# Optimization experiments

Measured on AMD Instinct MI355X. Metric: run time of the kernel, lower is better.

## Reference

```python
import jax, jax.numpy as jnp
import numpy as np

DEPTH, DIM, HEADS, DIM_HEAD, MLP = 6, 768, 12, 64, 3072
INNER = HEADS * DIM_HEAD  # 768
EPS = 1e-5


def _layernorm(x, w, b):
    m = jnp.mean(x, axis=-1, keepdims=True)
    v = jnp.mean((x - m) ** 2, axis=-1, keepdims=True)
    return (x - m) * jax.lax.rsqrt(v + EPS) * w + b


def setup_inputs() -> dict:
    key = jax.random.key(0)
    ks = jax.random.split(key, 12)
    s = 0.02
    return {
        "x": jax.random.normal(ks[0], (4, 1024, DIM), dtype=jnp.float32),
        "ln1_w": jnp.ones((DEPTH, DIM), jnp.float32),
        "ln1_b": jnp.zeros((DEPTH, DIM), jnp.float32),
        "w_qkv": jax.random.normal(ks[1], (DEPTH, DIM, 3 * INNER), jnp.float32) * s,
        "w_o": jax.random.normal(ks[2], (DEPTH, INNER, DIM), jnp.float32) * s,
        "b_o": jnp.zeros((DEPTH, DIM), jnp.float32),
        "ln2_w": jnp.ones((DEPTH, DIM), jnp.float32),
        "ln2_b": jnp.zeros((DEPTH, DIM), jnp.float32),
        "w1": jax.random.normal(ks[3], (DEPTH, DIM, MLP), jnp.float32) * s,
        "b1": jnp.zeros((DEPTH, MLP), jnp.float32),
        "w2": jax.random.normal(ks[4], (DEPTH, MLP, DIM), jnp.float32) * s,
        "b2": jnp.zeros((DEPTH, DIM), jnp.float32),
    }


def _forward(x, ln1_w, ln1_b, w_qkv, w_o, b_o, ln2_w, ln2_b, w1, b1, w2, b2):
    scale = DIM_HEAD ** -0.5
    b, n, _ = x.shape

    def block(x, p):
        l1w, l1b, wqkv, wo, bo, l2w, l2b, W1, B1, W2, B2 = p
        # --- attention (pre-norm); dropout/droppath are identity in eval ---
        h = _layernorm(x, l1w, l1b)
        qkv = h @ wqkv                                   # [b, n, 3*inner]
        q, k, v = jnp.split(qkv, 3, axis=-1)
        q = q.reshape(b, n, HEADS, DIM_HEAD).transpose(0, 2, 1, 3)
        k = k.reshape(b, n, HEADS, DIM_HEAD).transpose(0, 2, 1, 3)
        v = v.reshape(b, n, HEADS, DIM_HEAD).transpose(0, 2, 1, 3)
        dots = jnp.einsum('bhid,bhjd->bhij', q, k) * scale   # [b, h, n, n]
        attn = jax.nn.softmax(dots, axis=-1)
        out = jnp.einsum('bhij,bhjd->bhid', attn, v)
        out = out.transpose(0, 2, 1, 3).reshape(b, n, INNER)
        x = x + out @ wo + bo
        # --- feed-forward (pre-norm), exact GELU like torch default ---
        h = _layernorm(x, l2w, l2b)
        x = x + jax.nn.gelu(h @ W1 + B1, approximate=False) @ W2 + B2
        return x, None

    x, _ = jax.lax.scan(block, x, (ln1_w, ln1_b, w_qkv, w_o, b_o,
                                   ln2_w, ln2_b, w1, b1, w2, b2))
    return x


def reference(x, ln1_w, ln1_b, w_qkv, w_o, b_o, ln2_w, ln2_b, w1, b1, w2, b2):
    return _forward(x, ln1_w, ln1_b, w_qkv, w_o, b_o, ln2_w, ln2_b, w1, b1, w2, b2)
```

## Files before the change

### kernel.cpp

```cpp
#include <hip/hip_runtime.h>
#include <cmath>
#include <cstdint>

typedef __bf16 bf16_t;
typedef __bf16 bf16x8 __attribute__((ext_vector_type(8)));
typedef __bf16 bf16x4 __attribute__((ext_vector_type(4)));
typedef float  f32x4  __attribute__((ext_vector_type(4)));

#define DEPTH 6
#define DIM   768
#define HEADS 12
#define DH    64
#define MLPD  3072
#define SEQ   1024
#define BATCH 4
#define MTOT  (BATCH*SEQ)
#define QKVN  2304

static __device__ __forceinline__ bf16x8 ld8(const bf16_t* p) {
    return *(const bf16x8*)p;
}

typedef const __attribute__((address_space(1))) unsigned int gas_u32;
typedef __attribute__((address_space(3))) unsigned int las_u32;
static __device__ __forceinline__ void gload16(const bf16_t* g, bf16_t* l) {
    __builtin_amdgcn_global_load_lds((gas_u32*)g, (las_u32*)l, 16, 0, 0);
}

__global__ __launch_bounds__(256) void tcvt_kernel(const float* __restrict__ in,
                                                   bf16_t* __restrict__ out,
                                                   int K, int N) {
    __shared__ float ts[32][33];
    int n0 = blockIdx.x * 32, k0 = blockIdx.y * 32;
    size_t base = (size_t)blockIdx.z * K * N;
    int tx = threadIdx.x & 31, ty = threadIdx.x >> 5;
    #pragma unroll
    for (int r = 0; r < 32; r += 8)
        ts[ty + r][tx] = in[base + (size_t)(k0 + ty + r) * N + n0 + tx];
    __syncthreads();
    #pragma unroll
    for (int r = 0; r < 32; r += 8)
        out[base + (size_t)(n0 + ty + r) * K + k0 + tx] = (bf16_t)ts[tx][ty + r];
}

__global__ __launch_bounds__(192) void lnr_kernel(const float* __restrict__ xin,
                                                  float* __restrict__ xout,
                                                  const float* __restrict__ P,
                                                  int nslices,
                                                  const float* __restrict__ bias,
                                                  const float* __restrict__ w,
                                                  const float* __restrict__ b,
                                                  bf16_t* __restrict__ h,
                                                  int writeLN) {
    int row = blockIdx.x, t = threadIdx.x;
    size_t r4 = (size_t)row * 192 + t;
    float4 v = ((const float4*)xin)[r4];
    if (nslices) {
        float4 bi = ((const float4*)bias)[t];
        v.x += bi.x; v.y += bi.y; v.z += bi.z; v.w += bi.w;
        for (int s = 0; s < nslices; s++) {
            float4 pv = ((const float4*)P)[(size_t)s * MTOT * 192 + r4];
            v.x += pv.x; v.y += pv.y; v.z += pv.z; v.w += pv.w;
        }
        ((float4*)xout)[r4] = v;
    }
    float s = v.x + v.y + v.z + v.w;
    float q = v.x * v.x + v.y * v.y + v.z * v.z + v.w * v.w;
    #pragma unroll
    for (int off = 32; off > 0; off >>= 1) {
        s += __shfl_down(s, off);
        q += __shfl_down(q, off);
    }
    __shared__ float ss[3], sq[3], stat[2];
    if ((t & 63) == 0) { ss[t >> 6] = s; sq[t >> 6] = q; }
    __syncthreads();
    if (t == 0) {
        float S = ss[0] + ss[1] + ss[2];
        float Q = sq[0] + sq[1] + sq[2];
        float mean = S * (1.0f / DIM);
        float var  = Q * (1.0f / DIM) - mean * mean;
        stat[0] = mean;
        stat[1] = rsqrtf(var + 1e-5f);
    }
    __syncthreads();
    if (writeLN) {
        float mean = stat[0], rstd = stat[1];
        float4 wv4 = ((const float4*)w)[t];
        float4 bv4 = ((const float4*)b)[t];
        bf16x4 o;
        o[0] = (bf16_t)((v.x - mean) * rstd * wv4.x + bv4.x);
        o[1] = (bf16_t)((v.y - mean) * rstd * wv4.y + bv4.y);
        o[2] = (bf16_t)((v.z - mean) * rstd * wv4.z + bv4.z);
        o[3] = (bf16_t)((v.w - mean) * rstd * wv4.w + bv4.w);
        *(bf16x4*)&h[(size_t)row * DIM + t * 4] = o;
    }
}

template <int EPI>
__global__ __launch_bounds__(256) void gemm_kernel(const bf16_t* __restrict__ A,
                                                   const bf16_t* __restrict__ Bt,
                                                   const float* __restrict__ bias,
                                                   bf16_t* __restrict__ Cb,
                                                   float* __restrict__ Cf,
                                                   bf16_t* __restrict__ Vt,
                                                   int N, int K, int klen) {
    __shared__ __align__(16) bf16_t As[2][128 * 32];
    __shared__ __align__(16) bf16_t Bs[2][128 * 32];
    int t = threadIdx.x;
    int m0 = blockIdx.y * 128, n0 = blockIdx.x * 128;
    int kz = blockIdx.z;
    int kbeg = kz * klen;
    int lane = t & 63, l16 = lane & 15, quad = lane >> 4;
    int wv = t >> 6, wm = wv >> 1, wn = wv & 1;
    f32x4 acc[4][4] = {};

    int sr = lane >> 2;
    int sc = ((lane & 3) ^ ((lane >> 3) & 3)) * 8;
    const bf16_t* gA0 = A  + (size_t)(m0 + wv * 32 + sr) * K + sc;
    const bf16_t* gA1 = gA0 + (size_t)16 * K;
    const bf16_t* gB0 = Bt + (size_t)(n0 + wv * 32 + sr) * K + sc;
    const bf16_t* gB1 = gB0 + (size_t)16 * K;
    bf16_t* lA0 = &As[0][(wv * 32) * 32];
    bf16_t* lA1 = &As[0][(wv * 32 + 16) * 32];
    bf16_t* lB0 = &Bs[0][(wv * 32) * 32];
    bf16_t* lB1 = &Bs[0][(wv * 32 + 16) * 32];
    const int bufoff = 128 * 32;

    auto stage = [&](int buf, int k0) {
        gload16(gA0 + k0, lA0 + buf * bufoff);
        gload16(gA1 + k0, lA1 + buf * bufoff);
        gload16(gB0 + k0, lB0 + buf * bufoff);
        gload16(gB1 + k0, lB1 + buf * bufoff);
    };

    int nIt = klen >> 5;
    stage(0, kbeg);
    int posA = (quad ^ ((l16 >> 1) & 3)) * 8;

    for (int it = 0; it < nIt; it++) {
        __syncthreads();
        if (it + 1 < nIt) stage((it + 1) & 1, kbeg + (it + 1) * 32);
        const bf16_t* as = As[it & 1];
        const bf16_t* bs = Bs[it & 1];
        bf16x8 af[4], bfr[4];
        #pragma unroll
        for (int i = 0; i < 4; i++)
            af[i] = ld8(&as[(wm * 64 + i * 16 + l16) * 32 + posA]);
        #pragma unroll
        for (int j = 0; j < 4; j++)
            bfr[j] = ld8(&bs[(wn * 64 + j * 16 + l16) * 32 + posA]);
        #pragma unroll
        for (int i = 0; i < 4; i++)
            #pragma unroll
            for (int j = 0; j < 4; j++)
                acc[i][j] = __builtin_amdgcn_mfma_f32_16x16x32_bf16(af[i], bfr[j], acc[i][j], 0, 0, 0);
    }

    if constexpr (EPI == 0) {
        if (n0 >= 1536) {
            int b = m0 >> 10;
            #pragma unroll
            for (int i = 0; i < 4; i++) {
                int n = (m0 & 1023) + wm * 64 + i * 16 + quad * 4;
                #pragma unroll
                for (int j = 0; j < 4; j++) {
                    int hc = n0 + wn * 64 + j * 16 + l16 - 1536;
                    int hh = hc >> 6, d = hc & 63;
                    bf16x4 ov;
                    #pragma unroll
                    for (int r = 0; r < 4; r++) ov[r] = (bf16_t)acc[i][j][r];
                    *(bf16x4*)&Vt[(((size_t)b * HEADS + hh) * 64 + d) * SEQ + n] = ov;
                }
            }
            return;
        }
    }
    #pragma unroll
    for (int i = 0; i < 4; i++) {
        int grow = m0 + wm * 64 + i * 16 + quad * 4;
        #pragma unroll
        for (int j = 0; j < 4; j++) {
            int gcol = n0 + wn * 64 + j * 16 + l16;
            float bv = 0.0f;
            if constexpr (EPI == 1) bv = bias[gcol];
            #pragma unroll
            for (int r = 0; r < 4; r++) {
                size_t idx = (size_t)(grow + r) * N + gcol;
                float v = acc[i][j][r];
                if constexpr (EPI == 0) {
                    Cb[idx] = (bf16_t)v;
                } else if constexpr (EPI == 1) {
                    v += bv;
                    v = 0.5f * v * (1.0f + erff(v * 0.70710678118654752f));
                    Cb[idx] = (bf16_t)v;
                } else {
                    Cf[(size_t)kz * MTOT * N + idx] = v;
                }
            }
        }
    }
}

__global__ __launch_bounds__(256) void attn_kernel(const bf16_t* __restrict__ qkv,
                                                   const bf16_t* __restrict__ vt,
                                                   bf16_t* __restrict__ out) {
    int qt = blockIdx.x, h = blockIdx.y, b = blockIdx.z;
    int t = threadIdx.x;
    int wv = t >> 6, lane = t & 63, l16 = lane & 15, quad = lane >> 4;
    const float LOG2E = 1.44269504f;
    int qw0 = qt * 64 + wv * 16;

    __shared__ __align__(16) bf16_t Ks[2][64 * 64];
    __shared__ __align__(16) bf16_t Vs[2][64 * 64];
    __shared__ __align__(16) bf16_t Pa[4][16 * 72];
    bf16_t* P = Pa[wv];

    size_t bS = (size_t)b * SEQ;
    const bf16_t* qrow = qkv + (bS + qw0 + l16) * QKVN + h * 64;
    bf16x8 qf0 = ld8(qrow + quad * 8);
    bf16x8 qf1 = ld8(qrow + 32 + quad * 8);

    float m = -3e38f, l = 0.0f;
    f32x4 o[4] = {};

    const bf16_t* kbase = qkv + bS * QKVN + 768 + h * 64;
    const bf16_t* vbase = vt + ((size_t)(b * HEADS + h) * 64) * SEQ;

    int ar = lane >> 3;
    int ac = ((lane & 7) ^ ar) * 8;
    int i0 = wv * 2, i1 = wv * 2 + 1;
    const bf16_t* gK0 = kbase + (size_t)(i0 * 8 + ar) * QKVN + ac;
    const bf16_t* gK1 = kbase + (size_t)(i1 * 8 + ar) * QKVN + ac;
    const bf16_t* gV0 = vbase + (size_t)(i0 * 8 + ar) * SEQ + ac;
    const bf16_t* gV1 = vbase + (size_t)(i1 * 8 + ar) * SEQ + ac;

    auto stage = [&](int buf, int kb) {
        gload16(gK0 + (size_t)kb * QKVN, &Ks[buf][i0 * 8 * 64]);
        gload16(gK1 + (size_t)kb * QKVN, &Ks[buf][i1 * 8 * 64]);
        gload16(gV0 + kb, &Vs[buf][i0 * 8 * 64]);
        gload16(gV1 + kb, &Vs[buf][i1 * 8 * 64]);
    };

    stage(0, 0);
    int p0 = (quad ^ (l16 & 7)) * 8;
    int p1 = ((quad + 4) ^ (l16 & 7)) * 8;

    for (int it = 0; it < SEQ / 64; it++) {
        __syncthreads();
        if (it + 1 < SEQ / 64) stage((it + 1) & 1, (it + 1) * 64);
        const bf16_t* ks = Ks[it & 1];
        const bf16_t* vs = Vs[it & 1];

        f32x4 s[4];
        #pragma unroll
        for (int tt = 0; tt < 4; tt++) {
            const bf16_t* kr = &ks[(tt * 16 + l16) * 64];
            f32x4 z = {};
            z = __builtin_amdgcn_mfma_f32_16x16x32_bf16(ld8(kr + p0), qf0, z, 0, 0, 0);
            z = __builtin_amdgcn_mfma_f32_16x16x32_bf16(ld8(kr + p1), qf1, z, 0, 0, 0);
            s[tt] = z;
        }
        float mx = -3e38f;
        #pragma unroll
        for (int tt = 0; tt < 4; tt++)
            #pragma unroll
            for (int r = 0; r < 4; r++) {
                s[tt][r] *= 0.125f;
                mx = fmaxf(mx, s[tt][r]);
            }
        mx = fmaxf(mx, __shfl_xor(mx, 16));
        mx = fmaxf(mx, __shfl_xor(mx, 32));
        float mn = fmaxf(m, mx);
        float alpha = exp2f((m - mn) * LOG2E);
        m = mn;
        float nb = mn * LOG2E;
        float rs = 0.0f;
        #pragma unroll
        for (int tt = 0; tt < 4; tt++) {
            bf16x4 pkt;
            #pragma unroll
            for (int r = 0; r < 4; r++) {
                float p = exp2f(fmaf(s[tt][r], LOG2E, -nb));
                rs += p;
                pkt[r] = (bf16_t)p;
            }
            *(bf16x4*)&P[l16 * 72 + tt * 16 + quad * 4] = pkt;
        }
        l = l * alpha + rs;
        #pragma unroll
        for (int jt = 0; jt < 4; jt++) o[jt] *= alpha;
        asm volatile("s_waitcnt lgkmcnt(0)" ::: "memory");
        bf16x8 pf0 = ld8(&P[l16 * 72 + quad * 8]);
        bf16x8 pf1 = ld8(&P[l16 * 72 + 32 + quad * 8]);
        #pragma unroll
        for (int jt = 0; jt < 4; jt++) {
            const bf16_t* vr = &vs[(jt * 16 + l16) * 64];
            o[jt] = __builtin_amdgcn_mfma_f32_16x16x32_bf16(ld8(vr + p0), pf0, o[jt], 0, 0, 0);
            o[jt] = __builtin_amdgcn_mfma_f32_16x16x32_bf16(ld8(vr + p1), pf1, o[jt], 0, 0, 0);
        }
    }

    l += __shfl_xor(l, 16);
    l += __shfl_xor(l, 32);
    float inv = 1.0f / l;
    bf16_t* orow = out + (bS + qw0 + l16) * DIM + h * 64;
    #pragma unroll
    for (int jt = 0; jt < 4; jt++) {
        bf16x4 ov;
        #pragma unroll
        for (int r = 0; r < 4; r++) ov[r] = (bf16_t)(o[jt][r] * inv);
        *(bf16x4*)&orow[jt * 16 + quad * 4] = ov;
    }
}

extern "C" void kernel_launch(void* const* d_in, const int* in_sizes, int n_in,
                              void* d_out, int out_size, void* d_ws, size_t ws_size,
                              hipStream_t stream) {
    const float* x     = (const float*)d_in[0];
    const float* ln1_w = (const float*)d_in[1];
    const float* ln1_b = (const float*)d_in[2];
    const float* w_qkv = (const float*)d_in[3];
    const float* w_o   = (const float*)d_in[4];
    const float* b_o   = (const float*)d_in[5];
    const float* ln2_w = (const float*)d_in[6];
    const float* ln2_b = (const float*)d_in[7];
    const float* w1    = (const float*)d_in[8];
    const float* b1    = (const float*)d_in[9];
    const float* w2    = (const float*)d_in[10];
    const float* b2    = (const float*)d_in[11];
    float* out = (float*)d_out;

    char* ws = (char*)d_ws;
    size_t off = 0;
    auto alloc = [&](size_t bytes) -> char* {
        char* p = ws + off;
        off += (bytes + 255) & ~(size_t)255;
        return p;
    };
    bf16_t* wqkv_t = (bf16_t*)alloc((size_t)DEPTH * DIM * QKVN * 2);
    bf16_t* wo_t   = (bf16_t*)alloc((size_t)DEPTH * DIM * DIM * 2);
    bf16_t* w1_t   = (bf16_t*)alloc((size_t)DEPTH * DIM * MLPD * 2);
    bf16_t* w2_t   = (bf16_t*)alloc((size_t)DEPTH * MLPD * DIM * 2);
    bf16_t* hbuf   = (bf16_t*)alloc((size_t)MTOT * DIM * 2);
    bf16_t* qkvb   = (bf16_t*)alloc((size_t)MTOT * QKVN * 2);
    bf16_t* vtb    = (bf16_t*)alloc((size_t)BATCH * HEADS * 64 * SEQ * 2);
    bf16_t* aob    = (bf16_t*)alloc((size_t)MTOT * DIM * 2);
    bf16_t* midb   = (bf16_t*)alloc((size_t)MTOT * MLPD * 2);
    float*  Pm     = (float*)alloc((size_t)4 * MTOT * DIM * 4);
    float*  Pp     = (float*)qkvb;
    if (off > ws_size) return;

    tcvt_kernel<<<dim3(QKVN / 32, DIM / 32, DEPTH), 256, 0, stream>>>(w_qkv, wqkv_t, DIM, QKVN);
    tcvt_kernel<<<dim3(DIM / 32,  DIM / 32, DEPTH), 256, 0, stream>>>(w_o,   wo_t,   DIM, DIM);
    tcvt_kernel<<<dim3(MLPD / 32, DIM / 32, DEPTH), 256, 0, stream>>>(w1,    w1_t,   DIM, MLPD);
    tcvt_kernel<<<dim3(DIM / 32, MLPD / 32, DEPTH), 256, 0, stream>>>(w2,    w2_t,   MLPD, DIM);

    hipMemcpyAsync(out, x, (size_t)MTOT * DIM * 4, hipMemcpyDeviceToDevice, stream);

    lnr_kernel<<<MTOT, 192, 0, stream>>>(out, out, nullptr, 0, nullptr,
                                         ln1_w, ln1_b, hbuf, 1);

    for (int L = 0; L < DEPTH; L++) {
        gemm_kernel<0><<<dim3(QKVN / 128, MTOT / 128, 1), 256, 0, stream>>>(
            hbuf, wqkv_t + (size_t)L * DIM * QKVN, nullptr, qkvb, nullptr, vtb,
            QKVN, DIM, DIM);
        attn_kernel<<<dim3(SEQ / 64, HEADS, BATCH), 256, 0, stream>>>(qkvb, vtb, aob);
        gemm_kernel<2><<<dim3(DIM / 128, MTOT / 128, 2), 256, 0, stream>>>(
            aob, wo_t + (size_t)L * DIM * DIM, nullptr, nullptr, Pp, nullptr,
            DIM, DIM, 384);
        lnr_kernel<<<MTOT, 192, 0, stream>>>(out, out, Pp, 2, b_o + L * DIM,
                                             ln2_w + L * DIM, ln2_b + L * DIM, hbuf, 1);
        gemm_kernel<1><<<dim3(MLPD / 128, MTOT / 128, 1), 256, 0, stream>>>(
            hbuf, w1_t + (size_t)L * DIM * MLPD, b1 + L * MLPD, midb, nullptr, nullptr,
            MLPD, DIM, DIM);
        gemm_kernel<2><<<dim3(DIM / 128, MTOT / 128, 4), 256, 0, stream>>>(
            midb, w2_t + (size_t)L * MLPD * DIM, nullptr, nullptr, Pm, nullptr,
            DIM, MLPD, 768);
        if (L < DEPTH - 1) {
            lnr_kernel<<<MTOT, 192, 0, stream>>>(out, out, Pm, 4, b2 + L * DIM,
                                                 ln1_w + (L + 1) * DIM,
                                                 ln1_b + (L + 1) * DIM, hbuf, 1);
        } else {
            lnr_kernel<<<MTOT, 192, 0, stream>>>(out, out, Pm, 4, b2 + L * DIM,
                                                 ln1_w, ln1_b, hbuf, 0);
        }
    }
}
```

Measured before the change: 1.289 ms.

## Triple-buffer GEMM LDS pipeline and use 128x64 tiles for smaller GEMMs

The GEMM kernel moves from double to triple buffering. Loads are issued two stages ahead, and explicit vmcnt waits plus a raw s_barrier replace __syncthreads, so global loads overlap more compute. A BN template parameter adds a 128x64 tile variant, used for the QKV, out-projection and FF1 GEMMs to double the workgroup count on the many-CU GPU. The out-projection partials now go to the Pm buffer instead of aliasing qkvb. The smaller tiles lower data reuse per block, and the tuned waitcnt counts must match the number of loads issued per stage.

```diff
diff --git a/kernel.cpp b/kernel.cpp
--- a/kernel.cpp
+++ b/kernel.cpp
@@ -96,7 +96,7 @@
     }
 }
 
-template <int EPI>
+template <int EPI, int BN>
 __global__ __launch_bounds__(256) void gemm_kernel(const bf16_t* __restrict__ A,
                                                    const bf16_t* __restrict__ Bt,
                                                    const float* __restrict__ bias,
@@ -104,55 +104,65 @@
                                                    float* __restrict__ Cf,
                                                    bf16_t* __restrict__ Vt,
                                                    int N, int K, int klen) {
-    __shared__ __align__(16) bf16_t As[2][128 * 32];
-    __shared__ __align__(16) bf16_t Bs[2][128 * 32];
+    constexpr int NJ = BN / 32;
+    __shared__ __align__(16) bf16_t As[3][128 * 32];
+    __shared__ __align__(16) bf16_t Bs[3][BN * 32];
     int t = threadIdx.x;
-    int m0 = blockIdx.y * 128, n0 = blockIdx.x * 128;
+    int m0 = blockIdx.y * 128, n0 = blockIdx.x * BN;
     int kz = blockIdx.z;
     int kbeg = kz * klen;
     int lane = t & 63, l16 = lane & 15, quad = lane >> 4;
     int wv = t >> 6, wm = wv >> 1, wn = wv & 1;
-    f32x4 acc[4][4] = {};
+    f32x4 acc[4][NJ] = {};
 
     int sr = lane >> 2;
     int sc = ((lane & 3) ^ ((lane >> 3) & 3)) * 8;
     const bf16_t* gA0 = A  + (size_t)(m0 + wv * 32 + sr) * K + sc;
     const bf16_t* gA1 = gA0 + (size_t)16 * K;
-    const bf16_t* gB0 = Bt + (size_t)(n0 + wv * 32 + sr) * K + sc;
+    const bf16_t* gB0 = Bt + (size_t)(n0 + wv * (BN == 128 ? 32 : 16) + sr) * K + sc;
     const bf16_t* gB1 = gB0 + (size_t)16 * K;
     bf16_t* lA0 = &As[0][(wv * 32) * 32];
     bf16_t* lA1 = &As[0][(wv * 32 + 16) * 32];
-    bf16_t* lB0 = &Bs[0][(wv * 32) * 32];
+    bf16_t* lB0 = &Bs[0][(wv * (BN == 128 ? 32 : 16)) * 32];
     bf16_t* lB1 = &Bs[0][(wv * 32 + 16) * 32];
-    const int bufoff = 128 * 32;
+    constexpr int bufA = 128 * 32;
+    constexpr int bufB = BN * 32;
 
     auto stage = [&](int buf, int k0) {
-        gload16(gA0 + k0, lA0 + buf * bufoff);
-        gload16(gA1 + k0, lA1 + buf * bufoff);
-        gload16(gB0 + k0, lB0 + buf * bufoff);
-        gload16(gB1 + k0, lB1 + buf * bufoff);
+        gload16(gA0 + k0, lA0 + buf * bufA);
+        gload16(gA1 + k0, lA1 + buf * bufA);
+        gload16(gB0 + k0, lB0 + buf * bufB);
+        if constexpr (BN == 128) gload16(gB1 + k0, lB1 + buf * bufB);
     };
 
     int nIt = klen >> 5;
     stage(0, kbeg);
+    if (nIt > 1) stage(1, kbeg + 32);
     int posA = (quad ^ ((l16 >> 1) & 3)) * 8;
 
     for (int it = 0; it < nIt; it++) {
-        __syncthreads();
-        if (it + 1 < nIt) stage((it + 1) & 1, kbeg + (it + 1) * 32);
-        const bf16_t* as = As[it & 1];
-        const bf16_t* bs = Bs[it & 1];
-        bf16x8 af[4], bfr[4];
+        if (it + 1 < nIt) {
+            if constexpr (BN == 128) asm volatile("s_waitcnt vmcnt(4)" ::: "memory");
+            else                     asm volatile("s_waitcnt vmcnt(3)" ::: "memory");
+        } else {
+            asm volatile("s_waitcnt vmcnt(0)" ::: "memory");
+        }
+        __builtin_amdgcn_s_barrier();
+        asm volatile("" ::: "memory");
+        if (it + 2 < nIt) stage((it + 2) % 3, kbeg + (it + 2) * 32);
+        const bf16_t* as = As[it % 3];
+        const bf16_t* bs = Bs[it % 3];
+        bf16x8 af[4], bfr[NJ];
         #pragma unroll
         for (int i = 0; i < 4; i++)
             af[i] = ld8(&as[(wm * 64 + i * 16 + l16) * 32 + posA]);
         #pragma unroll
-        for (int j = 0; j < 4; j++)
-            bfr[j] = ld8(&bs[(wn * 64 + j * 16 + l16) * 32 + posA]);
+        for (int j = 0; j < NJ; j++)
+            bfr[j] = ld8(&bs[(wn * (16 * NJ) + j * 16 + l16) * 32 + posA]);
         #pragma unroll
         for (int i = 0; i < 4; i++)
             #pragma unroll
-            for (int j = 0; j < 4; j++)
+            for (int j = 0; j < NJ; j++)
                 acc[i][j] = __builtin_amdgcn_mfma_f32_16x16x32_bf16(af[i], bfr[j], acc[i][j], 0, 0, 0);
     }
 
@@ -163,8 +173,8 @@
             for (int i = 0; i < 4; i++) {
                 int n = (m0 & 1023) + wm * 64 + i * 16 + quad * 4;
                 #pragma unroll
-                for (int j = 0; j < 4; j++) {
-                    int hc = n0 + wn * 64 + j * 16 + l16 - 1536;
+                for (int j = 0; j < NJ; j++) {
+                    int hc = n0 + wn * (16 * NJ) + j * 16 + l16 - 1536;
                     int hh = hc >> 6, d = hc & 63;
                     bf16x4 ov;
                     #pragma unroll
@@ -179,8 +189,8 @@
     for (int i = 0; i < 4; i++) {
         int grow = m0 + wm * 64 + i * 16 + quad * 4;
         #pragma unroll
-        for (int j = 0; j < 4; j++) {
-            int gcol = n0 + wn * 64 + j * 16 + l16;
+        for (int j = 0; j < NJ; j++) {
+            int gcol = n0 + wn * (16 * NJ) + j * 16 + l16;
             float bv = 0.0f;
             if constexpr (EPI == 1) bv = bias[gcol];
             #pragma unroll
@@ -347,7 +357,7 @@
     bf16_t* aob    = (bf16_t*)alloc((size_t)MTOT * DIM * 2);
     bf16_t* midb   = (bf16_t*)alloc((size_t)MTOT * MLPD * 2);
     float*  Pm     = (float*)alloc((size_t)4 * MTOT * DIM * 4);
-    float*  Pp     = (float*)qkvb;
+    float*  Pp     = Pm;
     if (off > ws_size) return;
 
     tcvt_kernel<<<dim3(QKVN / 32, DIM / 32, DEPTH), 256, 0, stream>>>(w_qkv, wqkv_t, DIM, QKVN);
@@ -361,19 +371,19 @@
                                          ln1_w, ln1_b, hbuf, 1);
 
     for (int L = 0; L < DEPTH; L++) {
-        gemm_kernel<0><<<dim3(QKVN / 128, MTOT / 128, 1), 256, 0, stream>>>(
+        gemm_kernel<0, 64><<<dim3(QKVN / 64, MTOT / 128, 1), 256, 0, stream>>>(
             hbuf, wqkv_t + (size_t)L * DIM * QKVN, nullptr, qkvb, nullptr, vtb,
             QKVN, DIM, DIM);
         attn_kernel<<<dim3(SEQ / 64, HEADS, BATCH), 256, 0, stream>>>(qkvb, vtb, aob);
-        gemm_kernel<2><<<dim3(DIM / 128, MTOT / 128, 2), 256, 0, stream>>>(
+        gemm_kernel<2, 64><<<dim3(DIM / 64, MTOT / 128, 2), 256, 0, stream>>>(
             aob, wo_t + (size_t)L * DIM * DIM, nullptr, nullptr, Pp, nullptr,
             DIM, DIM, 384);
         lnr_kernel<<<MTOT, 192, 0, stream>>>(out, out, Pp, 2, b_o + L * DIM,
                                              ln2_w + L * DIM, ln2_b + L * DIM, hbuf, 1);
-        gemm_kernel<1><<<dim3(MLPD / 128, MTOT / 128, 1), 256, 0, stream>>>(
+        gemm_kernel<1, 64><<<dim3(MLPD / 64, MTOT / 128, 1), 256, 0, stream>>>(
             hbuf, w1_t + (size_t)L * DIM * MLPD, b1 + L * MLPD, midb, nullptr, nullptr,
             MLPD, DIM, DIM);
-        gemm_kernel<2><<<dim3(DIM / 128, MTOT / 128, 4), 256, 0, stream>>>(
+        gemm_kernel<2, 128><<<dim3(DIM / 128, MTOT / 128, 4), 256, 0, stream>>>(
             midb, w2_t + (size_t)L * MLPD * DIM, nullptr, nullptr, Pm, nullptr,
             DIM, MLPD, 768);
         if (L < DEPTH - 1) {
```

Result: slower. 1.388 ms (+7.7%).
